# Performance work log

Measured on AMD Instinct MI355X. Metric: run time of the kernel, lower is better.

## Reference

```python
import jax, jax.numpy as jnp
import numpy as np

MARGIN = 0.3
BIG = 1e5  # same constant the torch code uses to mask out same-id entries for the min


def setup_inputs() -> dict:
    key = jax.random.key(0)
    k1, k2, k3 = jax.random.split(key, 3)
    B, D, N_LUT, N_ID = 4096, 1024, 5000, 1024
    feat = jax.random.normal(k1, (B, D), dtype=jnp.float32)
    lut = jax.random.normal(k2, (N_LUT, D), dtype=jnp.float32)
    id = jax.random.randint(k3, (B,), 0, N_ID, dtype=jnp.int64)
    return {"feat": feat, "lut": lut, "id": id}


def reference(feat, lut, id):
    # feat_oim = lut[id]  (gather rows of the OIM lookup table)
    feat_oim = lut[id]  # (B, D)

    # Pairwise euclidean distance dist[i,j] = sqrt(||feat_i - feat_oim_j||^2 + 1e-12)
    # via the dot-product trick (avoids materializing the (B,B,D) diff tensor).
    sq_a = jnp.sum(feat * feat, axis=1)          # (B,)
    sq_b = jnp.sum(feat_oim * feat_oim, axis=1)  # (B,)
    sq = sq_a[:, None] + sq_b[None, :] - 2.0 * (feat @ feat_oim.T)  # (B, B)
    dist = jnp.sqrt(jnp.maximum(sq, 0.0) + 1e-12)

    # Masks (mode='id'):
    same_id = id[:, None] == id[None, :]               # (B, B) bool
    eye = jnp.eye(feat.shape[0], dtype=bool)
    positive_mask = same_id & ~eye

    # Batch-hard mining (n_dis=0):
    max_positive = jnp.max(dist * positive_mask.astype(dist.dtype), axis=1)   # hardest positive
    min_negative = jnp.min(dist + BIG * same_id.astype(dist.dtype), axis=1)   # hardest negative
    z = max_positive - min_negative

    # float margin path: hinge
    b_loss = jnp.maximum(z + MARGIN, 0.0)  # (B,)
    return b_loss
```

## Files before the change

### kernel.cpp

```cpp
#include <hip/hip_runtime.h>
#include <hip/hip_bf16.h>

#define B_N    4096
#define D_K    1024
#define N_C    1024
#define MARGIN 0.3f

typedef __attribute__((ext_vector_type(8))) short short8;
typedef __attribute__((ext_vector_type(4))) float f32x4;

__device__ inline ushort f2bf(float f) {
    unsigned u = __float_as_uint(f);
    unsigned r = (u + 0x7fffu + ((u >> 16) & 1u)) >> 16;
    return (ushort)r;
}

__device__ inline void async16(const ushort* g, ushort* l) {
    __builtin_amdgcn_global_load_lds(
        (const __attribute__((address_space(1))) void*)g,
        (__attribute__((address_space(3))) void*)l,
        16, 0, 0);
}

__global__ void prep_all(const float* __restrict__ feat,
                         const float* __restrict__ lut,
                         const int* __restrict__ id,
                         ushort* __restrict__ featB, ushort* __restrict__ lutB,
                         float* __restrict__ sq_a, float* __restrict__ sq_b,
                         int* __restrict__ cnt,
                         int* __restrict__ maxb, int* __restrict__ minb) {
    int b = blockIdx.x;
    int t = threadIdx.x;

    if (b == B_N + N_C) {
        __shared__ int hc[N_C];
        #pragma unroll
        for (int i = 0; i < 4; i++) hc[t * 4 + i] = 0;
        __syncthreads();
        #pragma unroll
        for (int i = 0; i < 16; i++) atomicAdd(&hc[id[t * 16 + i]], 1);
        __syncthreads();
        #pragma unroll
        for (int i = 0; i < 4; i++) cnt[t * 4 + i] = hc[t * 4 + i];
        return;
    }

    if (b < 16) {
        int i = b * 256 + t;
        maxb[i] = 0;
        minb[i] = 0x7F800000;
    }
    const float* src; ushort* dst; float* sq;
    if (b < B_N) {
        src = feat + (size_t)b * D_K;
        dst = featB + (size_t)b * D_K;
        sq  = sq_a + b;
    } else {
        int c = b - B_N;
        src = lut + (size_t)c * D_K;
        dst = lutB + (size_t)c * D_K;
        sq  = sq_b + c;
    }
    float4 v = ((const float4*)src)[t];
    float ss = v.x * v.x + v.y * v.y + v.z * v.z + v.w * v.w;
    ushort4 bb;
    bb.x = f2bf(v.x); bb.y = f2bf(v.y); bb.z = f2bf(v.z); bb.w = f2bf(v.w);
    ((ushort4*)dst)[t] = bb;

    int lane = t & 63, w = t >> 6;
    #pragma unroll
    for (int o = 1; o < 64; o <<= 1) ss += __shfl_xor(ss, o);
    __shared__ float red[4];
    if (lane == 0) red[w] = ss;
    __syncthreads();
    if (t == 0) *sq = red[0] + red[1] + red[2] + red[3];
}

__global__ __launch_bounds__(256, 4)
void dist_kernel(const ushort* __restrict__ A, const ushort* __restrict__ Bm,
                 const float* __restrict__ sqa, const float* __restrict__ sqb,
                 const int* __restrict__ ids, const int* __restrict__ cnt,
                 int* __restrict__ maxb, int* __restrict__ minb) {
    __shared__ ushort lds_[2 * 8192];

    const int t = threadIdx.x;
    const int lane = t & 63;
    const int wid = t >> 6;
    const int wr = wid >> 1;
    const int wc = wid & 1;
    const int l15 = lane & 15;
    const int h = lane >> 4;
    const int wo = wid * 512;

    const int bid = blockIdx.y * gridDim.x + blockIdx.x;
    const int swz = (bid & 7) * 128 + (bid >> 3);
    const int rb = swz >> 4, cb = swz & 15;

    const ushort* gA[2]; const ushort* gB[2];
    #pragma unroll
    for (int q = 0; q < 2; q++) {
        int p = q * 2048 + t * 8;
        int r = p >> 6;
        int j = (p >> 3) & 7;
        int col = (j ^ (r & 7)) << 3;
        gA[q] = A  + (size_t)(rb * 64 + r) * D_K + col;
        gB[q] = Bm + (size_t)(cb * 64 + r) * D_K + col;
    }

    const int q7 = l15 & 7;
    int offA[2][2], offB[2][2];
    #pragma unroll
    for (int mf = 0; mf < 2; mf++)
        #pragma unroll
        for (int ks = 0; ks < 2; ks++) {
            offA[mf][ks] = (wr * 32 + mf * 16 + l15) * 64
                         + (((ks * 4 + h) ^ q7) << 3);
            offB[mf][ks] = (wc * 32 + mf * 16 + l15) * 64
                         + (((ks * 4 + h) ^ q7) << 3);
        }

    f32x4 acc[2][2] = {};

    async16(gA[0], lds_ + wo);
    async16(gA[1], lds_ + 2048 + wo);
    async16(gB[0], lds_ + 4096 + wo);
    async16(gB[1], lds_ + 4096 + 2048 + wo);

    for (int kt = 0; kt < 16; ++kt) {
        const int s = kt & 1;
        const ushort* sA = lds_ + s * 8192;
        const ushort* sB = sA + 4096;

        if (kt < 15) {
            ushort* wb = lds_ + (s ^ 1) * 8192;
            const int nc = (kt + 1) * 64;
            async16(gA[0] + nc, wb + wo);
            async16(gA[1] + nc, wb + 2048 + wo);
            async16(gB[0] + nc, wb + 4096 + wo);
            async16(gB[1] + nc, wb + 4096 + 2048 + wo);
            asm volatile("s_waitcnt vmcnt(4)" ::: "memory");
        } else {
            asm volatile("s_waitcnt vmcnt(0)" ::: "memory");
        }
        __builtin_amdgcn_sched_barrier(0);
        __builtin_amdgcn_s_barrier();
        __builtin_amdgcn_sched_barrier(0);

        short8 afv[2][2], bfv[2][2];
        #pragma unroll
        for (int mf = 0; mf < 2; mf++)
            #pragma unroll
            for (int ks = 0; ks < 2; ks++) {
                afv[mf][ks] = *(const short8*)(sA + offA[mf][ks]);
                bfv[mf][ks] = *(const short8*)(sB + offB[mf][ks]);
            }
        asm volatile("s_waitcnt lgkmcnt(0)" ::: "memory");
        __builtin_amdgcn_sched_barrier(0);
        __builtin_amdgcn_s_setprio(1);
        #pragma unroll
        for (int mf = 0; mf < 2; mf++)
            #pragma unroll
            for (int nf = 0; nf < 2; nf++)
                #pragma unroll
                for (int ks = 0; ks < 2; ks++)
                    acc[mf][nf] = __builtin_amdgcn_mfma_f32_16x16x32_bf16(
                        afv[mf][ks], bfv[nf][ks], acc[mf][nf], 0, 0, 0);
        __builtin_amdgcn_s_setprio(0);
        __builtin_amdgcn_sched_barrier(0);
        __builtin_amdgcn_s_barrier();
    }

    int colg[2]; float sb2[2]; int c2[2];
    #pragma unroll
    for (int nf = 0; nf < 2; nf++) {
        int c = cb * 64 + wc * 32 + nf * 16 + l15;
        colg[nf] = c; sb2[nf] = sqb[c]; c2[nf] = cnt[c];
    }
    #pragma unroll
    for (int m = 0; m < 2; m++) {
        #pragma unroll
        for (int r = 0; r < 4; r++) {
            int row = rb * 64 + wr * 32 + m * 16 + h * 4 + r;
            float sa = sqa[row];
            int ida = ids[row];
            float mx = 0.0f, mn = 3.0e38f;
            #pragma unroll
            for (int nf = 0; nf < 2; nf++) {
                float s2 = sa + sb2[nf] - 2.0f * acc[m][nf][r];
                float d = sqrtf(fmaxf(s2, 0.0f) + 1e-12f);
                bool iseq = (colg[nf] == ida);
                float pv = (iseq && c2[nf] >= 2) ? d : 0.0f;
                float nv = (c2[nf] > 0 && !iseq) ? d : 3.0e38f;
                mx = fmaxf(mx, pv);
                mn = fminf(mn, nv);
            }
            #pragma unroll
            for (int o = 1; o < 16; o <<= 1) {
                mx = fmaxf(mx, __shfl_xor(mx, o));
                mn = fminf(mn, __shfl_xor(mn, o));
            }
            if (l15 == 0) {
                atomicMax(maxb + row, __float_as_int(mx));
                atomicMin(minb + row, __float_as_int(mn));
            }
        }
    }
}

__global__ void finalize_k(const int* __restrict__ maxb, const int* __restrict__ minb,
                           float* __restrict__ out) {
    int i = blockIdx.x * blockDim.x + threadIdx.x;
    if (i < B_N) {
        float z = __int_as_float(maxb[i]) - __int_as_float(minb[i]) + MARGIN;
        out[i] = fmaxf(z, 0.0f);
    }
}

extern "C" void kernel_launch(void* const* d_in, const int* in_sizes, int n_in,
                              void* d_out, int out_size, void* d_ws, size_t ws_size,
                              hipStream_t stream) {
    const float* feat = (const float*)d_in[0];
    const float* lut  = (const float*)d_in[1];
    const int*   id   = (const int*)d_in[2];
    float* out = (float*)d_out;

    char* ws = (char*)d_ws;
    ushort* featB = (ushort*)ws;
    ushort* lutB  = (ushort*)(ws + (size_t)B_N * D_K * 2);
    float*  sq_a  = (float*)(ws + (size_t)(B_N + N_C) * D_K * 2);
    float*  sq_b  = sq_a + B_N;
    int*    cnt   = (int*)(sq_b + N_C);
    int*    maxb  = cnt + N_C;
    int*    minb  = maxb + B_N;

    prep_all<<<B_N + N_C + 1, 256, 0, stream>>>(feat, lut, id, featB, lutB,
                                                sq_a, sq_b, cnt, maxb, minb);

    dim3 grid(N_C / 64, B_N / 64);
    dist_kernel<<<grid, 256, 0, stream>>>(featB, lutB, sq_a, sq_b, id, cnt,
                                          maxb, minb);

    finalize_k<<<16, 256, 0, stream>>>(maxb, minb, out);
}
```

Measured before the change: 34.44 us.

## Triple-buffer LDS tiles in dist_kernel and drop the second per-iteration barrier

Moves the GEMM main loop from double- to triple-buffered LDS staging. Two k-tiles are prefetched up front and each iteration issues the load two tiles ahead, so only one workgroup barrier per iteration is needed, before the reads. The explicit lgkmcnt wait and its sched barriers are removed and left to the compiler. LDS per block grows by half and launch bounds drop from 4 to 3 blocks per CU, which trades occupancy for deeper prefetch and fewer barriers.

```diff
diff --git a/kernel.cpp b/kernel.cpp
--- a/kernel.cpp
+++ b/kernel.cpp
@@ -76,12 +76,12 @@
     if (t == 0) *sq = red[0] + red[1] + red[2] + red[3];
 }
 
-__global__ __launch_bounds__(256, 4)
+__global__ __launch_bounds__(256, 3)
 void dist_kernel(const ushort* __restrict__ A, const ushort* __restrict__ Bm,
                  const float* __restrict__ sqa, const float* __restrict__ sqb,
                  const int* __restrict__ ids, const int* __restrict__ cnt,
                  int* __restrict__ maxb, int* __restrict__ minb) {
-    __shared__ ushort lds_[2 * 8192];
+    __shared__ ushort lds_[3 * 8192];
 
     const int t = threadIdx.x;
     const int lane = t & 63;
@@ -121,30 +121,35 @@
 
     f32x4 acc[2][2] = {};
 
-    async16(gA[0], lds_ + wo);
-    async16(gA[1], lds_ + 2048 + wo);
-    async16(gB[0], lds_ + 4096 + wo);
-    async16(gB[1], lds_ + 4096 + 2048 + wo);
-
+    #pragma unroll
+    for (int kt0 = 0; kt0 < 2; kt0++) {
+        ushort* base = lds_ + kt0 * 8192;
+        const int nc = kt0 * 64;
+        async16(gA[0] + nc, base + wo);
+        async16(gA[1] + nc, base + 2048 + wo);
+        async16(gB[0] + nc, base + 4096 + wo);
+        async16(gB[1] + nc, base + 4096 + 2048 + wo);
+    }
+
+    int s3 = 0, w3 = 2;
     for (int kt = 0; kt < 16; ++kt) {
-        const int s = kt & 1;
-        const ushort* sA = lds_ + s * 8192;
+        const ushort* sA = lds_ + s3 * 8192;
         const ushort* sB = sA + 4096;
 
-        if (kt < 15) {
-            ushort* wb = lds_ + (s ^ 1) * 8192;
-            const int nc = (kt + 1) * 64;
+        if (kt < 15) asm volatile("s_waitcnt vmcnt(4)" ::: "memory");
+        else         asm volatile("s_waitcnt vmcnt(0)" ::: "memory");
+        __builtin_amdgcn_sched_barrier(0);
+        __builtin_amdgcn_s_barrier();
+        __builtin_amdgcn_sched_barrier(0);
+
+        if (kt < 14) {
+            ushort* wb = lds_ + w3 * 8192;
+            const int nc = (kt + 2) * 64;
             async16(gA[0] + nc, wb + wo);
             async16(gA[1] + nc, wb + 2048 + wo);
             async16(gB[0] + nc, wb + 4096 + wo);
             async16(gB[1] + nc, wb + 4096 + 2048 + wo);
-            asm volatile("s_waitcnt vmcnt(4)" ::: "memory");
-        } else {
-            asm volatile("s_waitcnt vmcnt(0)" ::: "memory");
         }
-        __builtin_amdgcn_sched_barrier(0);
-        __builtin_amdgcn_s_barrier();
-        __builtin_amdgcn_sched_barrier(0);
 
         short8 afv[2][2], bfv[2][2];
         #pragma unroll
@@ -154,8 +159,6 @@
                 afv[mf][ks] = *(const short8*)(sA + offA[mf][ks]);
                 bfv[mf][ks] = *(const short8*)(sB + offB[mf][ks]);
             }
-        asm volatile("s_waitcnt lgkmcnt(0)" ::: "memory");
-        __builtin_amdgcn_sched_barrier(0);
         __builtin_amdgcn_s_setprio(1);
         #pragma unroll
         for (int mf = 0; mf < 2; mf++)
@@ -166,8 +169,9 @@
                     acc[mf][nf] = __builtin_amdgcn_mfma_f32_16x16x32_bf16(
                         afv[mf][ks], bfv[nf][ks], acc[mf][nf], 0, 0, 0);
         __builtin_amdgcn_s_setprio(0);
-        __builtin_amdgcn_sched_barrier(0);
-        __builtin_amdgcn_s_barrier();
+
+        s3 = (s3 == 2) ? 0 : s3 + 1;
+        w3 = (w3 == 2) ? 0 : w3 + 1;
     }
 
     int colg[2]; float sb2[2]; int c2[2];
```

Result: slower. 40.21 us (+16.7%).
